# Optimization experiments

Hardware: AMD Instinct MI355X
Metric: run time of the kernel (lower is better)

The kernel has to match this reference:

```python
import jax, jax.numpy as jnp
import numpy as np

K = 3  # dynamic filter kernel size
EPS = 1e-10


def _filter_norm_spatial(s, std_param):
    # s: (B, K*K, H, W); normalize over filter-tap dim (unbiased std, as torch)
    s = s - s.mean(axis=1, keepdims=True)
    s = s / (s.std(axis=1, keepdims=True, ddof=1) + EPS)
    return s * std_param[None, :, None, None]


def _filter_norm_channel(cf, std_param, B, C):
    # cf: (B, C*K*K); normalize over the K*K taps of each channel
    cf = cf.reshape(B, C, K * K)
    cf = cf - cf.mean(axis=2, keepdims=True)
    cf = cf / (cf.std(axis=2, keepdims=True, ddof=1) + EPS)
    cf = cf.reshape(B, C * K * K) * std_param[None, :]
    return cf.reshape(B, C, K * K)


def _ddf_pack(x, sw, sb, sstd, cw1, cb1, cw2, cb2, cstd):
    B, C, H, W = x.shape
    # spatial branch: 1x1 conv -> per-pixel K*K spatial filter
    s = jnp.einsum('bchw,oc->bohw', x, sw) + sb[None, :, None, None]
    s = _filter_norm_spatial(s, sstd)                      # (B, 9, H, W)
    # channel branch: GAP -> SE MLP -> per-channel K*K filter
    g = x.mean(axis=(2, 3))                                # (B, C)
    h = jax.nn.relu(g @ cw1.T + cb1)                       # (B, mid)
    cf = h @ cw2.T + cb2                                   # (B, C*9)
    cf = _filter_norm_channel(cf, cstd, B, C)              # (B, C, 9)
    # apply decoupled dynamic filter: w[b,c,uv,h,w] = cf[b,c,uv] * s[b,uv,h,w]
    pad = K // 2
    xp = jnp.pad(x, ((0, 0), (0, 0), (pad, pad), (pad, pad)))
    # patches: (B, C, 9, H, W) -- the 9 shifted views (unfold)
    patches = jnp.stack([xp[:, :, i:i + H, j:j + W]
                         for i in range(K) for j in range(K)], axis=2)
    return jnp.einsum('bckhw,bck,bkhw->bchw', patches, cf, s)


def setup_inputs() -> dict:
    key = jax.random.key(0)
    ks = jax.random.split(key, 20)
    nf, mid = 64, 12
    std_scale = np.sqrt(2.0) / K  # calculate_gain('relu') / kernel_size
    d = {'x': jax.random.normal(ks[0], (4, nf, 256, 256), jnp.float32)}
    i = 1
    for p in ('1', '2'):
        d['sw' + p] = jax.random.normal(ks[i], (K * K, nf), jnp.float32) * 0.1; i += 1
        d['sb' + p] = jax.random.normal(ks[i], (K * K,), jnp.float32) * 0.1; i += 1
        d['sstd' + p] = jax.random.normal(ks[i], (K * K,), jnp.float32) * std_scale; i += 1
        d['cw1_' + p] = jax.random.normal(ks[i], (mid, nf), jnp.float32) * 0.1; i += 1
        d['cb1_' + p] = jax.random.normal(ks[i], (mid,), jnp.float32) * 0.1; i += 1
        d['cw2_' + p] = jax.random.normal(ks[i], (nf * K * K, mid), jnp.float32) * 0.1; i += 1
        d['cb2_' + p] = jax.random.normal(ks[i], (nf * K * K,), jnp.float32) * 0.1; i += 1
        d['cstd' + p] = jax.random.normal(ks[i], (nf * K * K,), jnp.float32) * std_scale; i += 1
    return d


def reference(x, sw1, sb1, sstd1, cw1_1, cb1_1, cw2_1, cb2_1, cstd1,
              sw2, sb2, sstd2, cw1_2, cb1_2, cw2_2, cb2_2, cstd2):
    out = _ddf_pack(x, sw1, sb1, sstd1, cw1_1, cb1_1, cw2_1, cb2_1, cstd1)
    out = jax.nn.relu(out)
    out = _ddf_pack(out, sw2, sb2, sstd2, cw1_2, cb1_2, cw2_2, cb2_2, cstd2)
    return x + out
```

## Files before the change

### kernel.cpp

```cpp
#include <hip/hip_runtime.h>

#define B_ 4
#define C_ 64
#define H_ 256
#define W_ 256
#define HW_ (H_*W_)
#define MID_ 12

__global__ __launch_bounds__(256) void gap_kernel(const float* __restrict__ in,
                                                  float* __restrict__ g) {
    int bc = blockIdx.x;
    const float4* p4 = (const float4*)(in + (size_t)bc * HW_);
    float sum = 0.f;
    for (int i = threadIdx.x; i < HW_ / 4; i += 256) {
        float4 v = p4[i];
        sum += (v.x + v.y) + (v.z + v.w);
    }
    __shared__ float red[256];
    red[threadIdx.x] = sum;
    __syncthreads();
    for (int s = 128; s > 0; s >>= 1) {
        if (threadIdx.x < s) red[threadIdx.x] += red[threadIdx.x + s];
        __syncthreads();
    }
    if (threadIdx.x == 0) g[bc] = red[0] * (1.0f / HW_);
}

__global__ __launch_bounds__(256) void cf_kernel(const float* __restrict__ g,
    const float* __restrict__ cw1, const float* __restrict__ cb1,
    const float* __restrict__ cw2, const float* __restrict__ cb2,
    const float* __restrict__ cstd, float* __restrict__ cf) {
    __shared__ float hsm[B_][MID_];
    int tid = threadIdx.x;
    if (tid < B_ * MID_) {
        int b = tid / MID_, m = tid % MID_;
        float acc = cb1[m];
        for (int c = 0; c < C_; ++c) acc = fmaf(g[b * C_ + c], cw1[m * C_ + c], acc);
        hsm[b][m] = fmaxf(acc, 0.f);
    }
    __syncthreads();
    int b = tid >> 6, c = tid & 63;
    float v[9];
    float mean = 0.f;
#pragma unroll
    for (int t = 0; t < 9; ++t) {
        int o = c * 9 + t;
        float acc = cb2[o];
#pragma unroll
        for (int m = 0; m < MID_; ++m) acc = fmaf(hsm[b][m], cw2[o * MID_ + m], acc);
        v[t] = acc;
        mean += acc;
    }
    mean *= (1.f / 9.f);
    float var = 0.f;
#pragma unroll
    for (int t = 0; t < 9; ++t) { float d = v[t] - mean; var += d * d; }
    float inv = 1.f / (sqrtf(var * (1.f / 8.f)) + 1e-10f);
#pragma unroll
    for (int t = 0; t < 9; ++t)
        cf[(b * C_ + c) * 9 + t] = (v[t] - mean) * inv * cstd[c * 9 + t];
}

template <bool RELU, bool RESID>
__global__ __launch_bounds__(256) void ddf_main(const float* __restrict__ in,
    const float* __restrict__ sw, const float* __restrict__ sb,
    const float* __restrict__ sstd, const float* __restrict__ cf,
    const float* __restrict__ resid, float* __restrict__ out) {
    const int tx = threadIdx.x & 63, ty = threadIdx.x >> 6;
    const int w = blockIdx.x * 64 + tx;
    const int h = blockIdx.y * 4 + ty;
    const int b = blockIdx.z;
    const float* xb = in + (size_t)b * C_ * HW_;

    float s[9];
#pragma unroll
    for (int t = 0; t < 9; ++t) s[t] = sb[t];
    {
        const float* xp = xb + h * W_ + w;
        for (int c = 0; c < C_; ++c) {
            float xv = xp[(size_t)c * HW_];
#pragma unroll
            for (int t = 0; t < 9; ++t) s[t] = fmaf(xv, sw[t * C_ + c], s[t]);
        }
    }
    float mean = 0.f;
#pragma unroll
    for (int t = 0; t < 9; ++t) mean += s[t];
    mean *= (1.f / 9.f);
    float var = 0.f;
#pragma unroll
    for (int t = 0; t < 9; ++t) { float d = s[t] - mean; var += d * d; }
    float inv = 1.f / (sqrtf(var * (1.f / 8.f)) + 1e-10f);
#pragma unroll
    for (int t = 0; t < 9; ++t) s[t] = (s[t] - mean) * inv * sstd[t];

    const bool rok0 = (h > 0), rok2 = (h < H_ - 1);
    const bool cok0 = (w > 0), cok2 = (w < W_ - 1);
    const float* cfb = cf + b * (C_ * 9);
    const size_t base = (size_t)h * W_ + w;
    const size_t bbase = (size_t)b * C_ * HW_ + base;
    for (int c = 0; c < C_; ++c) {
        const float* xc = xb + (size_t)c * HW_ + base;
        float acc = 0.f;
#pragma unroll
        for (int i = 0; i < 3; ++i) {
            const bool rok = (i == 0) ? rok0 : ((i == 2) ? rok2 : true);
#pragma unroll
            for (int j = 0; j < 3; ++j) {
                const bool cok = (j == 0) ? cok0 : ((j == 2) ? cok2 : true);
                float xv = (rok && cok) ? xc[(i - 1) * W_ + (j - 1)] : 0.f;
                acc = fmaf(xv, cfb[c * 9 + i * 3 + j] * s[i * 3 + j], acc);
            }
        }
        if (RELU) acc = fmaxf(acc, 0.f);
        size_t oidx = bbase + (size_t)c * HW_;
        if (RESID) acc += resid[oidx];
        out[oidx] = acc;
    }
}

extern "C" void kernel_launch(void* const* d_in, const int* in_sizes, int n_in,
                              void* d_out, int out_size, void* d_ws, size_t ws_size,
                              hipStream_t stream) {
    const float* x     = (const float*)d_in[0];
    const float* sw1   = (const float*)d_in[1];
    const float* sb1   = (const float*)d_in[2];
    const float* sstd1 = (const float*)d_in[3];
    const float* cw1_1 = (const float*)d_in[4];
    const float* cb1_1 = (const float*)d_in[5];
    const float* cw2_1 = (const float*)d_in[6];
    const float* cb2_1 = (const float*)d_in[7];
    const float* cstd1 = (const float*)d_in[8];
    const float* sw2   = (const float*)d_in[9];
    const float* sb2   = (const float*)d_in[10];
    const float* sstd2 = (const float*)d_in[11];
    const float* cw1_2 = (const float*)d_in[12];
    const float* cb1_2 = (const float*)d_in[13];
    const float* cw2_2 = (const float*)d_in[14];
    const float* cb2_2 = (const float*)d_in[15];
    const float* cstd2 = (const float*)d_in[16];

    const size_t n_out1 = (size_t)B_ * C_ * HW_;
    const size_t need = (n_out1 + 256 + B_ * C_ * 9) * sizeof(float);
    if (ws_size < need) return;

    float* out1 = (float*)d_ws;
    float* g    = out1 + n_out1;
    float* cfb  = g + 256;
    float* out  = (float*)d_out;

    dim3 grid(W_ / 64, H_ / 4, B_);

    gap_kernel<<<B_ * C_, 256, 0, stream>>>(x, g);
    cf_kernel<<<1, 256, 0, stream>>>(g, cw1_1, cb1_1, cw2_1, cb2_1, cstd1, cfb);
    ddf_main<true, false><<<grid, 256, 0, stream>>>(x, sw1, sb1, sstd1, cfb, nullptr, out1);

    gap_kernel<<<B_ * C_, 256, 0, stream>>>(out1, g);
    cf_kernel<<<1, 256, 0, stream>>>(g, cw1_2, cb1_2, cw2_2, cb2_2, cstd2, cfb);
    ddf_main<false, true><<<grid, 256, 0, stream>>>(out1, sw2, sb2, sstd2, cfb, x, out);
}
```

Before: 160.5 us.

## Fuse GAP and spatial-filter computation into producer passes, 2 pixels per thread

Replaces the separate GAP and combined spatial+apply kernels with a pipeline. A prep kernel computes the normalized spatial filter map plus per-block partial channel sums. The first apply pass also computes the next layer's spatial filters and GAP partials from its ReLU output, which avoids re-reading the intermediate tensor twice. Each thread handles two adjacent columns with float2 loads, and the second pass splits channels across two blocks for more parallelism. This costs extra workspace for the spatial maps and partial sums, and keeps the old path as a fallback.

```diff
diff --git a/kernel.cpp b/kernel.cpp
--- a/kernel.cpp
+++ b/kernel.cpp
@@ -6,6 +6,206 @@
 #define W_ 256
 #define HW_ (H_*W_)
 #define MID_ 12
+#define NPB_ 128
+
+__device__ __forceinline__ float wave_reduce64(float v) {
+#pragma unroll
+    for (int off = 32; off; off >>= 1) v += __shfl_xor(v, off, 64);
+    return v;
+}
+
+__device__ __forceinline__ void fnorm9(float* t9, const float* __restrict__ sstd) {
+    float mean = 0.f;
+#pragma unroll
+    for (int t = 0; t < 9; ++t) mean += t9[t];
+    mean *= (1.f / 9.f);
+    float var = 0.f;
+#pragma unroll
+    for (int t = 0; t < 9; ++t) { float d = t9[t] - mean; var += d * d; }
+    float inv = 1.f / (sqrtf(var * (1.f / 8.f)) + 1e-10f);
+#pragma unroll
+    for (int t = 0; t < 9; ++t) t9[t] = (t9[t] - mean) * inv * sstd[t];
+}
+
+__global__ __launch_bounds__(256) void prep_kernel(const float* __restrict__ x,
+    const float* __restrict__ sw, const float* __restrict__ sb,
+    const float* __restrict__ sstd, float* __restrict__ sarr, float* __restrict__ gp) {
+    const int tid = threadIdx.x;
+    const int lane = tid & 63, wv = tid >> 6;
+    const int col0 = (blockIdx.x * 64 + lane) * 2;
+    const int row  = blockIdx.y * 4 + wv;
+    const int b = blockIdx.z;
+    __shared__ float lg[4][C_];
+
+    float st0[9], st1[9];
+#pragma unroll
+    for (int t = 0; t < 9; ++t) { float bb = sb[t]; st0[t] = bb; st1[t] = bb; }
+
+    const float* xp = x + ((size_t)b * C_) * HW_ + (size_t)row * W_ + col0;
+    for (int c = 0; c < C_; ++c) {
+        float2 v = *(const float2*)(xp + (size_t)c * HW_);
+#pragma unroll
+        for (int t = 0; t < 9; ++t) {
+            float wt = sw[t * C_ + c];
+            st0[t] = fmaf(v.x, wt, st0[t]);
+            st1[t] = fmaf(v.y, wt, st1[t]);
+        }
+        float gs = wave_reduce64(v.x + v.y);
+        if (lane == 0) lg[wv][c] = gs;
+    }
+    fnorm9(st0, sstd);
+    fnorm9(st1, sstd);
+    {
+        float* sp = sarr + ((size_t)b * 9) * HW_ + (size_t)row * W_ + col0;
+#pragma unroll
+        for (int t = 0; t < 9; ++t)
+            *(float2*)(sp + (size_t)t * HW_) = make_float2(st0[t], st1[t]);
+    }
+    __syncthreads();
+    if (tid < C_) {
+        float s4 = lg[0][tid] + lg[1][tid] + lg[2][tid] + lg[3][tid];
+        gp[((size_t)b * C_ + tid) * NPB_ + blockIdx.y * gridDim.x + blockIdx.x] = s4;
+    }
+}
+
+__global__ __launch_bounds__(256) void cfk(const float* __restrict__ gp,
+    const float* __restrict__ cw1, const float* __restrict__ cb1,
+    const float* __restrict__ cw2, const float* __restrict__ cb2,
+    const float* __restrict__ cstd, float* __restrict__ cf) {
+    const int tid = threadIdx.x;
+    const int b = tid >> 6, c = tid & 63;
+    __shared__ float gsm[B_][C_];
+    __shared__ float hsm[B_][MID_];
+    {
+        const float4* p4 = (const float4*)(gp + ((size_t)b * C_ + c) * NPB_);
+        float s = 0.f;
+#pragma unroll
+        for (int i = 0; i < NPB_ / 4; ++i) { float4 v = p4[i]; s += (v.x + v.y) + (v.z + v.w); }
+        gsm[b][c] = s * (1.f / HW_);
+    }
+    __syncthreads();
+    if (tid < B_ * MID_) {
+        int b2 = tid / MID_, m = tid % MID_;
+        float a = cb1[m];
+        for (int cc = 0; cc < C_; ++cc) a = fmaf(gsm[b2][cc], cw1[m * C_ + cc], a);
+        hsm[b2][m] = fmaxf(a, 0.f);
+    }
+    __syncthreads();
+    float v[9];
+    float mean = 0.f;
+#pragma unroll
+    for (int t = 0; t < 9; ++t) {
+        int o = c * 9 + t;
+        float a = cb2[o];
+#pragma unroll
+        for (int m = 0; m < MID_; ++m) a = fmaf(hsm[b][m], cw2[o * MID_ + m], a);
+        v[t] = a;
+        mean += a;
+    }
+    mean *= (1.f / 9.f);
+    float var = 0.f;
+#pragma unroll
+    for (int t = 0; t < 9; ++t) { float d = v[t] - mean; var += d * d; }
+    float inv = 1.f / (sqrtf(var * (1.f / 8.f)) + 1e-10f);
+#pragma unroll
+    for (int t = 0; t < 9; ++t)
+        cf[((size_t)b * C_ + c) * 9 + t] = (v[t] - mean) * inv * cstd[c * 9 + t];
+}
+
+template<bool PASS1>
+__global__ __launch_bounds__(256) void apply_kernel(const float* __restrict__ in,
+    const float* __restrict__ sarr, const float* __restrict__ cf,
+    const float* __restrict__ swn, const float* __restrict__ sbn,
+    const float* __restrict__ sstdn, const float* __restrict__ resid,
+    float* __restrict__ out, float* __restrict__ snext, float* __restrict__ gpn) {
+    const int tid = threadIdx.x;
+    const int lane = tid & 63, wv = tid >> 6;
+    const int col0 = (blockIdx.x * 64 + lane) * 2;
+    const int row  = blockIdx.y * 4 + wv;
+    int b, c0, cN;
+    if (PASS1) { b = blockIdx.z; c0 = 0; cN = C_; }
+    else       { b = blockIdx.z >> 1; c0 = (blockIdx.z & 1) * (C_ / 2); cN = C_ / 2; }
+    __shared__ float lg[4][C_];
+
+    float s0[9], s1[9];
+    {
+        const float* sp = sarr + ((size_t)b * 9) * HW_ + (size_t)row * W_ + col0;
+#pragma unroll
+        for (int t = 0; t < 9; ++t) {
+            float2 v = *(const float2*)(sp + (size_t)t * HW_);
+            s0[t] = v.x; s1[t] = v.y;
+        }
+    }
+    float nt0[9], nt1[9];
+    if (PASS1) {
+#pragma unroll
+        for (int t = 0; t < 9; ++t) { float bb = sbn[t]; nt0[t] = bb; nt1[t] = bb; }
+    }
+
+    const bool rup = row > 0, rdn = row < H_ - 1;
+    const bool cl = col0 > 0, cr = (col0 + 2) < W_;
+    const size_t pix = (size_t)row * W_ + col0;
+    const float* base = in + ((size_t)b * C_ + c0) * HW_ + pix;
+    const float* cfb  = cf + ((size_t)b * C_ + c0) * 9;
+    float* outp = out + ((size_t)b * C_ + c0) * HW_ + pix;
+    const float* rbase = PASS1 ? nullptr : (resid + ((size_t)b * C_ + c0) * HW_ + pix);
+
+    for (int c = 0; c < cN; ++c) {
+        const float* p = base + (size_t)c * HW_;
+        float m[3][4];
+#pragma unroll
+        for (int dr = 0; dr < 3; ++dr) {
+            const float* rp = p + (dr - 1) * W_;
+            const bool rv = (dr == 0) ? rup : ((dr == 2) ? rdn : true);
+            float2 mid = rv ? *(const float2*)rp : make_float2(0.f, 0.f);
+            m[dr][1] = mid.x; m[dr][2] = mid.y;
+            m[dr][0] = (rv && cl) ? rp[-1] : 0.f;
+            m[dr][3] = (rv && cr) ? rp[2] : 0.f;
+        }
+        float acc0 = 0.f, acc1 = 0.f;
+#pragma unroll
+        for (int dr = 0; dr < 3; ++dr)
+#pragma unroll
+            for (int dc = 0; dc < 3; ++dc) {
+                const int t = dr * 3 + dc;
+                const float w = cfb[c * 9 + t];
+                acc0 = fmaf(m[dr][dc]     * s0[t], w, acc0);
+                acc1 = fmaf(m[dr][dc + 1] * s1[t], w, acc1);
+            }
+        float2 o;
+        if (PASS1) {
+            o.x = fmaxf(acc0, 0.f);
+            o.y = fmaxf(acc1, 0.f);
+#pragma unroll
+            for (int t = 0; t < 9; ++t) {
+                float wt = swn[t * C_ + c];
+                nt0[t] = fmaf(o.x, wt, nt0[t]);
+                nt1[t] = fmaf(o.y, wt, nt1[t]);
+            }
+            float gs = wave_reduce64(o.x + o.y);
+            if (lane == 0) lg[wv][c] = gs;
+        } else {
+            float2 rv = *(const float2*)(rbase + (size_t)c * HW_);
+            o.x = acc0 + rv.x;
+            o.y = acc1 + rv.y;
+        }
+        *(float2*)(outp + (size_t)c * HW_) = o;
+    }
+
+    if (PASS1) {
+        fnorm9(nt0, sstdn);
+        fnorm9(nt1, sstdn);
+        float* sp = snext + ((size_t)b * 9) * HW_ + pix;
+#pragma unroll
+        for (int t = 0; t < 9; ++t)
+            *(float2*)(sp + (size_t)t * HW_) = make_float2(nt0[t], nt1[t]);
+        __syncthreads();
+        if (tid < C_) {
+            float s4 = lg[0][tid] + lg[1][tid] + lg[2][tid] + lg[3][tid];
+            gpn[((size_t)b * C_ + tid) * NPB_ + blockIdx.y * gridDim.x + blockIdx.x] = s4;
+        }
+    }
+}
 
 __global__ __launch_bounds__(256) void gap_kernel(const float* __restrict__ in,
                                                   float* __restrict__ g) {
@@ -71,7 +271,6 @@
     const int h = blockIdx.y * 4 + ty;
     const int b = blockIdx.z;
     const float* xb = in + (size_t)b * C_ * HW_;
-
     float s[9];
 #pragma unroll
     for (int t = 0; t < 9; ++t) s[t] = sb[t];
@@ -93,7 +292,6 @@
     float inv = 1.f / (sqrtf(var * (1.f / 8.f)) + 1e-10f);
 #pragma unroll
     for (int t = 0; t < 9; ++t) s[t] = (s[t] - mean) * inv * sstd[t];
-
     const bool rok0 = (h > 0), rok2 = (h < H_ - 1);
     const bool cok0 = (w > 0), cok2 = (w < W_ - 1);
     const float* cfb = cf + b * (C_ * 9);
@@ -139,23 +337,46 @@
     const float* cw2_2 = (const float*)d_in[14];
     const float* cb2_2 = (const float*)d_in[15];
     const float* cstd2 = (const float*)d_in[16];
+    float* outp = (float*)d_out;
 
     const size_t n_out1 = (size_t)B_ * C_ * HW_;
-    const size_t need = (n_out1 + 256 + B_ * C_ * 9) * sizeof(float);
-    if (ws_size < need) return;
-
+    const size_t n_s    = (size_t)B_ * 9 * HW_;
+    const size_t n_cf   = (size_t)B_ * C_ * 9;
+    const size_t n_gp   = (size_t)B_ * C_ * NPB_;
+    const size_t need_new = (n_out1 + 2 * n_s + 2 * n_cf + 2 * n_gp) * sizeof(float);
+
+    if (ws_size >= need_new) {
+        float* out1 = (float*)d_ws;
+        float* s1   = out1 + n_out1;
+        float* s2   = s1 + n_s;
+        float* cf1  = s2 + n_s;
+        float* cf2  = cf1 + n_cf;
+        float* gp1  = cf2 + n_cf;
+        float* gp2  = gp1 + n_gp;
+
+        dim3 gmain(W_ / 128, H_ / 4, B_);
+        dim3 gmain2(W_ / 128, H_ / 4, B_ * 2);
+
+        prep_kernel<<<gmain, 256, 0, stream>>>(x, sw1, sb1, sstd1, s1, gp1);
+        cfk<<<1, 256, 0, stream>>>(gp1, cw1_1, cb1_1, cw2_1, cb2_1, cstd1, cf1);
+        apply_kernel<true><<<gmain, 256, 0, stream>>>(x, s1, cf1, sw2, sb2, sstd2,
+                                                      nullptr, out1, s2, gp2);
+        cfk<<<1, 256, 0, stream>>>(gp2, cw1_2, cb1_2, cw2_2, cb2_2, cstd2, cf2);
+        apply_kernel<false><<<gmain2, 256, 0, stream>>>(out1, s2, cf2, nullptr, nullptr,
+                                                        nullptr, x, outp, nullptr, nullptr);
+        return;
+    }
+
+    const size_t need_old = (n_out1 + 256 + n_cf) * sizeof(float);
+    if (ws_size < need_old) return;
     float* out1 = (float*)d_ws;
     float* g    = out1 + n_out1;
     float* cfb  = g + 256;
-    float* out  = (float*)d_out;
-
     dim3 grid(W_ / 64, H_ / 4, B_);
-
     gap_kernel<<<B_ * C_, 256, 0, stream>>>(x, g);
     cf_kernel<<<1, 256, 0, stream>>>(g, cw1_1, cb1_1, cw2_1, cb2_1, cstd1, cfb);
     ddf_main<true, false><<<grid, 256, 0, stream>>>(x, sw1, sb1, sstd1, cfb, nullptr, out1);
-
     gap_kernel<<<B_ * C_, 256, 0, stream>>>(out1, g);
     cf_kernel<<<1, 256, 0, stream>>>(g, cw1_2, cb1_2, cw2_2, cb2_2, cstd2, cfb);
-    ddf_main<false, true><<<grid, 256, 0, stream>>>(out1, sw2, sb2, sstd2, cfb, x, out);
-}
+    ddf_main<false, true><<<grid, 256, 0, stream>>>(out1, sw2, sb2, sstd2, cfb, x, outp);
+}
```

New measurement: 162.0 us. Within noise of the previous version (+0.9%).

## Fuse GAP and spatial-filter computation into producer kernels, removing separate passes

Applied to the files above, without the earlier changes.

Global average pooling moves out of its own kernel. It is now computed as per-block partial sums inside the kernel that already reads each pixel's channels. The spatial filter for pass 2 is computed in the pass-1 apply epilogue and stored to workspace. This removes two full reads of the 64-channel tensor: the separate GAP reads and the spatial-branch re-read in the apply kernel. The cost is writing and reading 9-plane spatial filter arrays and a larger workspace. Channel filters are padded to 12 floats for float4 loads, and the kernels get occupancy launch bounds.

```diff
diff --git a/kernel.cpp b/kernel.cpp
--- a/kernel.cpp
+++ b/kernel.cpp
@@ -6,116 +6,195 @@
 #define W_ 256
 #define HW_ (H_*W_)
 #define MID_ 12
-
-__global__ __launch_bounds__(256) void gap_kernel(const float* __restrict__ in,
-                                                  float* __restrict__ g) {
-    int bc = blockIdx.x;
-    const float4* p4 = (const float4*)(in + (size_t)bc * HW_);
-    float sum = 0.f;
-    for (int i = threadIdx.x; i < HW_ / 4; i += 256) {
-        float4 v = p4[i];
-        sum += (v.x + v.y) + (v.z + v.w);
-    }
-    __shared__ float red[256];
-    red[threadIdx.x] = sum;
+#define NPB_ 256
+
+__device__ __forceinline__ float wave_reduce64(float v) {
+#pragma unroll
+    for (int off = 32; off; off >>= 1) v += __shfl_xor(v, off, 64);
+    return v;
+}
+
+__device__ __forceinline__ void fnorm9(float* t9, const float* __restrict__ sstd) {
+    float mean = 0.f;
+#pragma unroll
+    for (int t = 0; t < 9; ++t) mean += t9[t];
+    mean *= (1.f / 9.f);
+    float var = 0.f;
+#pragma unroll
+    for (int t = 0; t < 9; ++t) { float d = t9[t] - mean; var += d * d; }
+    float inv = 1.f / (sqrtf(var * (1.f / 8.f)) + 1e-10f);
+#pragma unroll
+    for (int t = 0; t < 9; ++t) t9[t] = (t9[t] - mean) * inv * sstd[t];
+}
+
+__global__ __launch_bounds__(256, 4) void prep_kernel(const float* __restrict__ x,
+    const float* __restrict__ sw, const float* __restrict__ sb,
+    const float* __restrict__ sstd, float* __restrict__ sarr, float* __restrict__ gp) {
+    const int lane = threadIdx.x & 63, wv = threadIdx.x >> 6;
+    const int col = blockIdx.x * 64 + lane;
+    const int row = blockIdx.y * 4 + wv;
+    const int b = blockIdx.z;
+    const int bslot = blockIdx.y * gridDim.x + blockIdx.x;
+    __shared__ float lg[4][C_];
+
+    float st[9];
+#pragma unroll
+    for (int t = 0; t < 9; ++t) st[t] = sb[t];
+
+    const float* xp = x + ((size_t)b * C_) * HW_ + (size_t)row * W_ + col;
+#pragma unroll 8
+    for (int c = 0; c < C_; ++c) {
+        float v = xp[(size_t)c * HW_];
+#pragma unroll
+        for (int t = 0; t < 9; ++t) st[t] = fmaf(v, sw[t * C_ + c], st[t]);
+        float g = wave_reduce64(v);
+        if (lane == 0) lg[wv][c] = g;
+    }
+    fnorm9(st, sstd);
+    {
+        float* sp = sarr + ((size_t)b * 9) * HW_ + (size_t)row * W_ + col;
+#pragma unroll
+        for (int t = 0; t < 9; ++t) sp[(size_t)t * HW_] = st[t];
+    }
     __syncthreads();
-    for (int s = 128; s > 0; s >>= 1) {
-        if (threadIdx.x < s) red[threadIdx.x] += red[threadIdx.x + s];
-        __syncthreads();
-    }
-    if (threadIdx.x == 0) g[bc] = red[0] * (1.0f / HW_);
-}
-
-__global__ __launch_bounds__(256) void cf_kernel(const float* __restrict__ g,
+    if (threadIdx.x < C_) {
+        int c = threadIdx.x;
+        float s4 = lg[0][c] + lg[1][c] + lg[2][c] + lg[3][c];
+        gp[((size_t)b * C_ + c) * NPB_ + bslot] = s4;
+    }
+}
+
+__global__ __launch_bounds__(256) void cfk(const float* __restrict__ gp,
     const float* __restrict__ cw1, const float* __restrict__ cb1,
     const float* __restrict__ cw2, const float* __restrict__ cb2,
     const float* __restrict__ cstd, float* __restrict__ cf) {
+    const int tid = threadIdx.x;
+    const int b = tid >> 6, c = tid & 63;
+    __shared__ float gsm[B_][C_];
     __shared__ float hsm[B_][MID_];
-    int tid = threadIdx.x;
+    {
+        const float4* p4 = (const float4*)(gp + ((size_t)b * C_ + c) * NPB_);
+        float s = 0.f;
+#pragma unroll 4
+        for (int i = 0; i < NPB_ / 4; ++i) { float4 v = p4[i]; s += (v.x + v.y) + (v.z + v.w); }
+        gsm[b][c] = s * (1.f / HW_);
+    }
+    __syncthreads();
     if (tid < B_ * MID_) {
-        int b = tid / MID_, m = tid % MID_;
-        float acc = cb1[m];
-        for (int c = 0; c < C_; ++c) acc = fmaf(g[b * C_ + c], cw1[m * C_ + c], acc);
-        hsm[b][m] = fmaxf(acc, 0.f);
+        int b2 = tid / MID_, m = tid % MID_;
+        float a = cb1[m];
+        for (int cc = 0; cc < C_; ++cc) a = fmaf(gsm[b2][cc], cw1[m * C_ + cc], a);
+        hsm[b2][m] = fmaxf(a, 0.f);
     }
     __syncthreads();
-    int b = tid >> 6, c = tid & 63;
     float v[9];
     float mean = 0.f;
 #pragma unroll
     for (int t = 0; t < 9; ++t) {
         int o = c * 9 + t;
-        float acc = cb2[o];
-#pragma unroll
-        for (int m = 0; m < MID_; ++m) acc = fmaf(hsm[b][m], cw2[o * MID_ + m], acc);
-        v[t] = acc;
-        mean += acc;
+        float a = cb2[o];
+#pragma unroll
+        for (int m = 0; m < MID_; ++m) a = fmaf(hsm[b][m], cw2[o * MID_ + m], a);
+        v[t] = a;
+        mean += a;
     }
     mean *= (1.f / 9.f);
     float var = 0.f;
 #pragma unroll
     for (int t = 0; t < 9; ++t) { float d = v[t] - mean; var += d * d; }
     float inv = 1.f / (sqrtf(var * (1.f / 8.f)) + 1e-10f);
-#pragma unroll
-    for (int t = 0; t < 9; ++t)
-        cf[(b * C_ + c) * 9 + t] = (v[t] - mean) * inv * cstd[c * 9 + t];
-}
-
-template <bool RELU, bool RESID>
-__global__ __launch_bounds__(256) void ddf_main(const float* __restrict__ in,
-    const float* __restrict__ sw, const float* __restrict__ sb,
-    const float* __restrict__ sstd, const float* __restrict__ cf,
-    const float* __restrict__ resid, float* __restrict__ out) {
-    const int tx = threadIdx.x & 63, ty = threadIdx.x >> 6;
-    const int w = blockIdx.x * 64 + tx;
-    const int h = blockIdx.y * 4 + ty;
+    float* o12 = cf + ((size_t)b * C_ + c) * 12;
+#pragma unroll
+    for (int t = 0; t < 9; ++t) o12[t] = (v[t] - mean) * inv * cstd[c * 9 + t];
+    o12[9] = 0.f; o12[10] = 0.f; o12[11] = 0.f;
+}
+
+template<bool PASS1>
+__global__ __launch_bounds__(256, 4) void apply_kernel(const float* __restrict__ in,
+    const float* __restrict__ sarr, const float* __restrict__ cf,
+    const float* __restrict__ swn, const float* __restrict__ sbn,
+    const float* __restrict__ sstdn, const float* __restrict__ resid,
+    float* __restrict__ out, float* __restrict__ snext, float* __restrict__ gpn) {
+    const int lane = threadIdx.x & 63, wv = threadIdx.x >> 6;
+    const int col = blockIdx.x * 64 + lane;
+    const int row = blockIdx.y * 4 + wv;
     const int b = blockIdx.z;
-    const float* xb = in + (size_t)b * C_ * HW_;
-
-    float s[9];
-#pragma unroll
-    for (int t = 0; t < 9; ++t) s[t] = sb[t];
+    const int bslot = blockIdx.y * gridDim.x + blockIdx.x;
+    __shared__ float lg[4][C_];
+
+    float s0[9];
     {
-        const float* xp = xb + h * W_ + w;
-        for (int c = 0; c < C_; ++c) {
-            float xv = xp[(size_t)c * HW_];
-#pragma unroll
-            for (int t = 0; t < 9; ++t) s[t] = fmaf(xv, sw[t * C_ + c], s[t]);
+        const float* sp = sarr + ((size_t)b * 9) * HW_ + (size_t)row * W_ + col;
+#pragma unroll
+        for (int t = 0; t < 9; ++t) s0[t] = sp[(size_t)t * HW_];
+    }
+    float nt[9];
+    if (PASS1) {
+#pragma unroll
+        for (int t = 0; t < 9; ++t) nt[t] = sbn[t];
+    }
+
+    const bool rup = row > 0, rdn = row < H_ - 1;
+    const bool cl = col > 0, cr = col < W_ - 1;
+    const size_t pix = (size_t)row * W_ + col;
+    const float* base = in + ((size_t)b * C_) * HW_ + pix;
+    const float* cfb  = cf + ((size_t)b * C_) * 12;
+    float* outp = out + ((size_t)b * C_) * HW_ + pix;
+    const float* rb = PASS1 ? nullptr : (resid + ((size_t)b * C_) * HW_ + pix);
+
+#pragma unroll 4
+    for (int c = 0; c < C_; ++c) {
+        const float4* cfv = (const float4*)(cfb + (size_t)c * 12);
+        float4 ca = cfv[0], cb4 = cfv[1], cc4 = cfv[2];
+        const float cw9[9] = {ca.x, ca.y, ca.z, ca.w, cb4.x, cb4.y, cb4.z, cb4.w, cc4.x};
+        const float* p = base + (size_t)c * HW_;
+        const float* ru = p - W_;
+        const float* rd = p + W_;
+        float m00 = (rup && cl) ? ru[-1] : 0.f;
+        float m01 = rup ? ru[0] : 0.f;
+        float m02 = (rup && cr) ? ru[1] : 0.f;
+        float m10 = cl ? p[-1] : 0.f;
+        float m11 = p[0];
+        float m12 = cr ? p[1] : 0.f;
+        float m20 = (rdn && cl) ? rd[-1] : 0.f;
+        float m21 = rdn ? rd[0] : 0.f;
+        float m22 = (rdn && cr) ? rd[1] : 0.f;
+        float acc = 0.f;
+        acc = fmaf(m00 * s0[0], cw9[0], acc);
+        acc = fmaf(m01 * s0[1], cw9[1], acc);
+        acc = fmaf(m02 * s0[2], cw9[2], acc);
+        acc = fmaf(m10 * s0[3], cw9[3], acc);
+        acc = fmaf(m11 * s0[4], cw9[4], acc);
+        acc = fmaf(m12 * s0[5], cw9[5], acc);
+        acc = fmaf(m20 * s0[6], cw9[6], acc);
+        acc = fmaf(m21 * s0[7], cw9[7], acc);
+        acc = fmaf(m22 * s0[8], cw9[8], acc);
+        float o;
+        if (PASS1) {
+            o = fmaxf(acc, 0.f);
+#pragma unroll
+            for (int t = 0; t < 9; ++t) nt[t] = fmaf(o, swn[t * C_ + c], nt[t]);
+            float g = wave_reduce64(o);
+            if (lane == 0) lg[wv][c] = g;
+        } else {
+            o = acc + rb[(size_t)c * HW_];
         }
-    }
-    float mean = 0.f;
-#pragma unroll
-    for (int t = 0; t < 9; ++t) mean += s[t];
-    mean *= (1.f / 9.f);
-    float var = 0.f;
-#pragma unroll
-    for (int t = 0; t < 9; ++t) { float d = s[t] - mean; var += d * d; }
-    float inv = 1.f / (sqrtf(var * (1.f / 8.f)) + 1e-10f);
-#pragma unroll
-    for (int t = 0; t < 9; ++t) s[t] = (s[t] - mean) * inv * sstd[t];
-
-    const bool rok0 = (h > 0), rok2 = (h < H_ - 1);
-    const bool cok0 = (w > 0), cok2 = (w < W_ - 1);
-    const float* cfb = cf + b * (C_ * 9);
-    const size_t base = (size_t)h * W_ + w;
-    const size_t bbase = (size_t)b * C_ * HW_ + base;
-    for (int c = 0; c < C_; ++c) {
-        const float* xc = xb + (size_t)c * HW_ + base;
-        float acc = 0.f;
-#pragma unroll
-        for (int i = 0; i < 3; ++i) {
-            const bool rok = (i == 0) ? rok0 : ((i == 2) ? rok2 : true);
-#pragma unroll
-            for (int j = 0; j < 3; ++j) {
-                const bool cok = (j == 0) ? cok0 : ((j == 2) ? cok2 : true);
-                float xv = (rok && cok) ? xc[(i - 1) * W_ + (j - 1)] : 0.f;
-                acc = fmaf(xv, cfb[c * 9 + i * 3 + j] * s[i * 3 + j], acc);
-            }
+        outp[(size_t)c * HW_] = o;
+    }
+
+    if (PASS1) {
+        fnorm9(nt, sstdn);
+        {
+            float* sp = snext + ((size_t)b * 9) * HW_ + pix;
+#pragma unroll
+            for (int t = 0; t < 9; ++t) sp[(size_t)t * HW_] = nt[t];
         }
-        if (RELU) acc = fmaxf(acc, 0.f);
-        size_t oidx = bbase + (size_t)c * HW_;
-        if (RESID) acc += resid[oidx];
-        out[oidx] = acc;
+        __syncthreads();
+        if (threadIdx.x < C_) {
+            int c = threadIdx.x;
+            float s4 = lg[0][c] + lg[1][c] + lg[2][c] + lg[3][c];
+            gpn[((size_t)b * C_ + c) * NPB_ + bslot] = s4;
+        }
     }
 }
 
@@ -139,23 +218,30 @@
     const float* cw2_2 = (const float*)d_in[14];
     const float* cb2_2 = (const float*)d_in[15];
     const float* cstd2 = (const float*)d_in[16];
+    float* outp = (float*)d_out;
 
     const size_t n_out1 = (size_t)B_ * C_ * HW_;
-    const size_t need = (n_out1 + 256 + B_ * C_ * 9) * sizeof(float);
+    const size_t n_s    = (size_t)B_ * 9 * HW_;
+    const size_t n_cf   = (size_t)B_ * C_ * 12;
+    const size_t n_gp   = (size_t)B_ * C_ * NPB_;
+    const size_t need = (n_out1 + 2 * n_s + 2 * n_cf + 2 * n_gp) * sizeof(float);
     if (ws_size < need) return;
 
     float* out1 = (float*)d_ws;
-    float* g    = out1 + n_out1;
-    float* cfb  = g + 256;
-    float* out  = (float*)d_out;
-
-    dim3 grid(W_ / 64, H_ / 4, B_);
-
-    gap_kernel<<<B_ * C_, 256, 0, stream>>>(x, g);
-    cf_kernel<<<1, 256, 0, stream>>>(g, cw1_1, cb1_1, cw2_1, cb2_1, cstd1, cfb);
-    ddf_main<true, false><<<grid, 256, 0, stream>>>(x, sw1, sb1, sstd1, cfb, nullptr, out1);
-
-    gap_kernel<<<B_ * C_, 256, 0, stream>>>(out1, g);
-    cf_kernel<<<1, 256, 0, stream>>>(g, cw1_2, cb1_2, cw2_2, cb2_2, cstd2, cfb);
-    ddf_main<false, true><<<grid, 256, 0, stream>>>(out1, sw2, sb2, sstd2, cfb, x, out);
-}
+    float* s1   = out1 + n_out1;
+    float* s2   = s1 + n_s;
+    float* cf1  = s2 + n_s;
+    float* cf2  = cf1 + n_cf;
+    float* gp1  = cf2 + n_cf;
+    float* gp2  = gp1 + n_gp;
+
+    dim3 g(W_ / 64, H_ / 4, B_);
+
+    prep_kernel<<<g, 256, 0, stream>>>(x, sw1, sb1, sstd1, s1, gp1);
+    cfk<<<1, 256, 0, stream>>>(gp1, cw1_1, cb1_1, cw2_1, cb2_1, cstd1, cf1);
+    apply_kernel<true><<<g, 256, 0, stream>>>(x, s1, cf1, sw2, sb2, sstd2,
+                                              nullptr, out1, s2, gp2);
+    cfk<<<1, 256, 0, stream>>>(gp2, cw1_2, cb1_2, cw2_2, cb2_2, cstd2, cf2);
+    apply_kernel<false><<<g, 256, 0, stream>>>(out1, s2, cf2, nullptr, nullptr,
+                                               nullptr, x, outp, nullptr, nullptr);
+}
```

New measurement: 180.3 us. +12.4%, slower.
